# Kernel optimization log

Hardware: AMD Instinct MI355X
Metric: run time of the kernel (lower is better)

## Reference

```python
import jax, jax.numpy as jnp
import numpy as np

N = 100000      # nodes
E = 3200000     # directed edges
G = 1024        # graphs in batch


def setup_inputs() -> dict:
    key = jax.random.key(0)
    ks = jax.random.split(key, 12)
    x = jax.random.normal(ks[0], (N, 4), dtype=jnp.float32)
    edge_index = jax.random.randint(ks[1], (2, E), 0, N, dtype=jnp.int64)
    batch = jnp.sort(jax.random.randint(ks[2], (N,), 0, G, dtype=jnp.int64))
    s = 0.1
    return {
        'x': x, 'edge_index': edge_index, 'batch': batch,
        'W_emb': jax.random.normal(ks[3], (4, 1), jnp.float32) * s,
        'b_emb': jax.random.normal(ks[4], (4,), jnp.float32) * s,
        'W1': jax.random.normal(ks[5], (16, 7), jnp.float32) * s,
        'b1': jax.random.normal(ks[6], (16,), jnp.float32) * s,
        'W2': jax.random.normal(ks[7], (8, 16), jnp.float32) * s,
        'b2': jax.random.normal(ks[8], (8,), jnp.float32) * s,
        'W3': jax.random.normal(ks[9], (1, 8), jnp.float32) * s,
        'b3': jax.random.normal(ks[10], (1,), jnp.float32) * s,
    }


def _gcn_norm(edge_index, n):
    # add self-loops (PyG GCNConv default)
    loops = jnp.arange(n, dtype=edge_index.dtype)
    row = jnp.concatenate([edge_index[0], loops])  # source
    col = jnp.concatenate([edge_index[1], loops])  # target
    deg = jax.ops.segment_sum(jnp.ones_like(col, dtype=jnp.float32), col, num_segments=n)
    dinv = jnp.where(deg > 0, deg ** -0.5, 0.0)
    norm = dinv[row] * dinv[col]
    return row, col, norm


def _gcn_conv(h, W, b, row, col, norm, n):
    h = h @ W.T                                   # [n, out]
    msg = h[row] * norm[:, None]                  # gather + scale
    out = jax.ops.segment_sum(msg, col, num_segments=n)
    return out + b


def reference(x, edge_index, batch, W_emb, b_emb, W1, b1, W2, b2, W3, b3):
    row, col, norm = _gcn_norm(edge_index, N)
    atoms_vector = x[:, :1]
    atoms_xyz = x[:, 1:]
    one_hot_emb = atoms_vector @ W_emb.T + b_emb          # [N, 4]
    h = jnp.concatenate([one_hot_emb, atoms_xyz], axis=1) # [N, 7]
    h = jnp.tanh(_gcn_conv(h, W1, b1, row, col, norm, N)) # [N, 16]
    # dropout is identity in eval mode
    h = jnp.tanh(_gcn_conv(h, W2, b2, row, col, norm, N)) # [N, 8]
    # scatter-mean readout over graphs
    sums = jax.ops.segment_sum(h, batch, num_segments=G)
    cnts = jax.ops.segment_sum(jnp.ones((h.shape[0],), h.dtype), batch, num_segments=G)
    pooled = sums / jnp.maximum(cnts, 1.0)[:, None]       # [G, 8]
    return pooled @ W3.T + b3                             # [G, 1]
```

## Files before the change

### kernel.cpp

```cpp
#include <hip/hip_runtime.h>
#include <hip/hip_fp16.h>


constexpr int BLK  = 256;
constexpr int NPB  = 256;
constexpr int NBMX = 512;
constexpr int CAPB = 9216;
constexpr int PBLK = 512;
constexpr int CAPS = 6144;
constexpr int EPT  = 12;
constexpr int SBLK = 512;
constexpr int MAXIT = CAPB / SBLK;

__global__ void k_place(const int4* __restrict__ row4, const int4* __restrict__ col4,
                        int* __restrict__ bucketCnt, unsigned int* __restrict__ data,
                        int E, int NB) {
    __shared__ unsigned int stage[CAPS];
    __shared__ int pos[NBMX], sstart[NBMX], lbase[NBMX];
    __shared__ int wsum[8];
    int t = threadIdx.x;
    int lane = t & 63, w = t >> 6;
    int begin = blockIdx.x * CAPS;
    int end = min(E, begin + CAPS);
    int csize = end - begin;
    int q0 = begin >> 2, q1 = end >> 2;
    if (t < NBMX) pos[t] = 0;
    __syncthreads();
    unsigned int ent[EPT];
    int meta[EPT];
#pragma unroll
    for (int it = 0; it < EPT / 4; it++) {
        int i = q0 + t + it * PBLK;
        bool ok = i < q1;
        int4 c = ok ? col4[i] : make_int4(0, 0, 0, 0);
        int4 r = ok ? row4[i] : make_int4(0, 0, 0, 0);
#pragma unroll
        for (int k = 0; k < 4; k++) {
            int cc = ((const int*)&c)[k];
            int rr = ((const int*)&r)[k];
            int b = cc >> 8;
            int o = ok ? atomicAdd(&pos[b], 1) : 0;
            ent[it * 4 + k] = ((unsigned int)(cc & 255) << 17) | (unsigned int)rr;
            meta[it * 4 + k] = ok ? ((b << 13) | o) : -1;
        }
    }
    __syncthreads();
    int v = pos[t];
    int sc = v;
#pragma unroll
    for (int off = 1; off < 64; off <<= 1) {
        int o = __shfl_up(sc, off, 64);
        if (lane >= off) sc += o;
    }
    if (lane == 63) wsum[w] = sc;
    __syncthreads();
    int pre = 0;
#pragma unroll
    for (int i = 0; i < 8; i++) if (i < w) pre += wsum[i];
    int excl = sc + pre - v;
    sstart[t] = excl;
    lbase[t] = v ? atomicAdd(&bucketCnt[t], v) : 0;
    __syncthreads();
#pragma unroll
    for (int k = 0; k < EPT; k++) {
        int m = meta[k];
        if (m >= 0) stage[sstart[m >> 13] + (m & 0x1FFF)] = ent[k];
    }
    __syncthreads();
    for (int k = t; k < csize; k += PBLK) {
        int lo = 0, hi = NB - 1;
        while (lo < hi) { int m = (lo + hi + 1) >> 1; if (sstart[m] <= k) lo = m; else hi = m - 1; }
        data[(unsigned int)lo * CAPB + (unsigned int)(lbase[lo] + (k - sstart[lo]))] = stage[k];
    }
}

__global__ void k_sort_node1(unsigned int* __restrict__ data,
                             const int* __restrict__ bucketCnt,
                             const float4* __restrict__ x,
                             const float* __restrict__ Wemb, const float* __restrict__ bemb,
                             const float* __restrict__ W1,
                             int* __restrict__ rs, int* __restrict__ re,
                             float* __restrict__ dinv, uint4* __restrict__ u1q, int n) {
    __shared__ int pos[NPB], startl[NPB];
    __shared__ int wsum[4];
    int b = blockIdx.x;
    int t = threadIdx.x;
    int base = b * CAPB;
    int cnt = min(bucketCnt[b], CAPB);
    if (t < NPB) pos[t] = 0;
    __syncthreads();
    unsigned int ent[MAXIT];
    int off[MAXIT];
#pragma unroll
    for (int it = 0; it < MAXIT; it++) {
        int i = t + it * SBLK;
        if (i < cnt) {
            unsigned int p = data[base + i];
            int dloc = (int)(p >> 17);
            int o = atomicAdd(&pos[dloc], 1);
            ent[it] = p & 0x1FFFF;
            off[it] = (dloc << 14) | o;
        } else off[it] = -1;
    }
    __syncthreads();
    int node = b * NPB + t;
    float d = 0.0f;
    if (t < NPB) {
        int lane = t & 63, w = t >> 6;
        int v = pos[t];
        int sc = v;
#pragma unroll
        for (int o = 1; o < 64; o <<= 1) {
            int s = __shfl_up(sc, o, 64);
            if (lane >= o) sc += s;
        }
        if (lane == 63) wsum[w] = sc;
        __syncthreads();
        int pre = 0;
#pragma unroll
        for (int i = 0; i < 4; i++) if (i < w) pre += wsum[i];
        int excl = sc + pre - v;
        startl[t] = excl;
        if (node < n) {
            rs[node] = base + excl;
            re[node] = base + excl + v;
            d = rsqrtf((float)v + 1.0f);
            dinv[node] = d;
        }
    } else {
        __syncthreads();
    }
    __syncthreads();
#pragma unroll
    for (int it = 0; it < MAXIT; it++) {
        int m = off[it];
        if (m >= 0) data[base + startl[m >> 14] + (m & 0x3FFF)] = ent[it];
    }
    if (t < NPB && node < n) {
        float4 xi = x[node];
        float h0[7];
#pragma unroll
        for (int j = 0; j < 4; j++) h0[j] = xi.x * Wemb[j] + bemb[j];
        h0[4] = xi.y; h0[5] = xi.z; h0[6] = xi.w;
        float s[16];
#pragma unroll
        for (int f = 0; f < 16; f++) {
            float tt = 0.0f;
#pragma unroll
            for (int j = 0; j < 7; j++) tt += h0[j] * W1[f * 7 + j];
            s[f] = tt * d;
        }
        union { __half2 h2[8]; uint4 u4[2]; } pk;
#pragma unroll
        for (int q = 0; q < 8; q++) pk.h2[q] = __floats2half2_rn(s[2*q], s[2*q+1]);
        u1q[node * 2]     = pk.u4[0];
        u1q[node * 2 + 1] = pk.u4[1];
    }
}

__global__ void k_agg1(const unsigned int* __restrict__ sorted,
                       const int* __restrict__ rs, const int* __restrict__ re,
                       const uint4* __restrict__ u1q, const float* __restrict__ dinv,
                       const float* __restrict__ b1, const float* __restrict__ W2,
                       uint2* __restrict__ u2h, int n) {
    __shared__ float hbuf[128][17];
    int t = threadIdx.x;
    int nl = t >> 1;
    int j = t & 1;
    int node = blockIdx.x * 128 + nl;
    if (node < n) {
        int s = rs[node], e = re[node];
        float acc[8];
#pragma unroll
        for (int k = 0; k < 8; k++) acc[k] = 0.0f;
        int i = s;
        for (; i + 4 <= e; i += 4) {
            uint4 q0 = u1q[sorted[i]     * 2 + j];
            uint4 q1 = u1q[sorted[i + 1] * 2 + j];
            uint4 q2 = u1q[sorted[i + 2] * 2 + j];
            uint4 q3 = u1q[sorted[i + 3] * 2 + j];
            const __half2* p0 = (const __half2*)&q0;
            const __half2* p1 = (const __half2*)&q1;
            const __half2* p2 = (const __half2*)&q2;
            const __half2* p3 = (const __half2*)&q3;
#pragma unroll
            for (int k = 0; k < 4; k++) {
                float2 a0 = __half22float2(p0[k]);
                float2 a1 = __half22float2(p1[k]);
                float2 a2 = __half22float2(p2[k]);
                float2 a3 = __half22float2(p3[k]);
                acc[2*k]   += (a0.x + a1.x) + (a2.x + a3.x);
                acc[2*k+1] += (a0.y + a1.y) + (a2.y + a3.y);
            }
        }
        for (; i < e; i++) {
            uint4 q = u1q[sorted[i] * 2 + j];
            const __half2* p = (const __half2*)&q;
#pragma unroll
            for (int k = 0; k < 4; k++) {
                float2 a = __half22float2(p[k]);
                acc[2*k]   += a.x;
                acc[2*k+1] += a.y;
            }
        }
        uint4 qs = u1q[node * 2 + j];
        const __half2* ps = (const __half2*)&qs;
        float d = dinv[node];
#pragma unroll
        for (int k = 0; k < 4; k++) {
            float2 a = __half22float2(ps[k]);
            hbuf[nl][j*8 + 2*k]   = tanhf(d * (acc[2*k]   + a.x) + b1[j*8 + 2*k]);
            hbuf[nl][j*8 + 2*k+1] = tanhf(d * (acc[2*k+1] + a.y) + b1[j*8 + 2*k+1]);
        }
    }
    __syncthreads();
    if (node < n) {
        float d = dinv[node];
        float r[4];
#pragma unroll
        for (int gg = 0; gg < 4; gg++) {
            float tt = 0.0f;
#pragma unroll
            for (int k = 0; k < 16; k++) tt += hbuf[nl][k] * W2[(j*4 + gg) * 16 + k];
            r[gg] = tt * d;
        }
        union { __half2 h2[2]; uint2 u2; } pk;
        pk.h2[0] = __floats2half2_rn(r[0], r[1]);
        pk.h2[1] = __floats2half2_rn(r[2], r[3]);
        u2h[node * 2 + j] = pk.u2;
    }
}

__global__ void k_agg2(const unsigned int* __restrict__ sorted,
                       const int* __restrict__ rs, const int* __restrict__ re,
                       const uint4* __restrict__ u2q, const float* __restrict__ dinv,
                       const float* __restrict__ b2, uint4* __restrict__ h2q, int n) {
    int node = blockIdx.x * BLK + threadIdx.x;
    if (node >= n) return;
    int s = rs[node], e = re[node];
    float acc[8];
#pragma unroll
    for (int k = 0; k < 8; k++) acc[k] = 0.0f;
    int i = s;
    for (; i + 2 <= e; i += 2) {
        uint4 q0 = u2q[sorted[i]];
        uint4 q1 = u2q[sorted[i + 1]];
        const __half2* p0 = (const __half2*)&q0;
        const __half2* p1 = (const __half2*)&q1;
#pragma unroll
        for (int k = 0; k < 4; k++) {
            float2 a0 = __half22float2(p0[k]);
            float2 a1 = __half22float2(p1[k]);
            acc[2*k]   += a0.x + a1.x;
            acc[2*k+1] += a0.y + a1.y;
        }
    }
    if (i < e) {
        uint4 q = u2q[sorted[i]];
        const __half2* p = (const __half2*)&q;
#pragma unroll
        for (int k = 0; k < 4; k++) {
            float2 a = __half22float2(p[k]);
            acc[2*k]   += a.x;
            acc[2*k+1] += a.y;
        }
    }
    uint4 qs = u2q[node];
    const __half2* ps = (const __half2*)&qs;
    float d = dinv[node];
    union { __half2 h2[4]; uint4 u4; } pk;
#pragma unroll
    for (int k = 0; k < 4; k++) {
        float2 a = __half22float2(ps[k]);
        pk.h2[k] = __floats2half2_rn(tanhf(d * (acc[2*k]   + a.x) + b2[2*k]),
                                     tanhf(d * (acc[2*k+1] + a.y) + b2[2*k+1]));
    }
    h2q[node] = pk.u4;
}

__global__ void k_pool_out(const uint4* __restrict__ h2q, const int* __restrict__ batch,
                           const float* __restrict__ W3, const float* __restrict__ b3,
                           float* __restrict__ out, int n) {
    int g = blockIdx.x;
    int lane = threadIdx.x;
    int lo = 0, hi = n;
    while (lo < hi) { int m = (lo + hi) >> 1; if (batch[m] < g) lo = m + 1; else hi = m; }
    int start = lo;
    hi = n;
    while (lo < hi) { int m = (lo + hi) >> 1; if (batch[m] < g + 1) lo = m + 1; else hi = m; }
    int end = lo;

    float s[8];
#pragma unroll
    for (int f = 0; f < 8; f++) s[f] = 0.0f;
    for (int i = start + lane; i < end; i += 64) {
        uint4 q = h2q[i];
        const __half2* ph = (const __half2*)&q;
#pragma unroll
        for (int p = 0; p < 4; p++) {
            float2 a = __half22float2(ph[p]);
            s[2*p]   += a.x;
            s[2*p+1] += a.y;
        }
    }
#pragma unroll
    for (int off = 32; off >= 1; off >>= 1) {
#pragma unroll
        for (int f = 0; f < 8; f++) s[f] += __shfl_down(s[f], off, 64);
    }
    if (lane == 0) {
        float c = fmaxf((float)(end - start), 1.0f);
        float t = 0.0f;
#pragma unroll
        for (int f = 0; f < 8; f++) t += (s[f] / c) * W3[f];
        out[g] = t + b3[0];
    }
}

extern "C" void kernel_launch(void* const* d_in, const int* in_sizes, int n_in,
                              void* d_out, int out_size, void* d_ws, size_t ws_size,
                              hipStream_t stream) {
    const float* x    = (const float*)d_in[0];
    const int*   ei   = (const int*)d_in[1];
    const int*   batch= (const int*)d_in[2];
    const float* Wemb = (const float*)d_in[3];
    const float* bemb = (const float*)d_in[4];
    const float* W1   = (const float*)d_in[5];
    const float* b1   = (const float*)d_in[6];
    const float* W2   = (const float*)d_in[7];
    const float* b2   = (const float*)d_in[8];
    const float* W3   = (const float*)d_in[9];
    const float* b3   = (const float*)d_in[10];
    float* out = (float*)d_out;

    const int n = in_sizes[2];
    const int E = in_sizes[1] / 2;
    const int G = out_size;
    const int* row = ei;
    const int* col = ei + E;
    const int NB = (n + NPB - 1) / NPB;

    float* ws    = (float*)d_ws;
    float* dinv  = ws;
    uint4* u1q   = (uint4*)(ws + n);
    __half* u2h  = (__half*)(ws + 9 * n);
    __half* h2h  = (__half*)(ws + 13 * n);
    int* rs      = (int*)(ws + 17 * n);
    int* re      = rs + n;
    int* bucketCnt = re + n;
    unsigned int* data = (unsigned int*)(bucketCnt + NBMX);

    int gridP = (E + CAPS - 1) / CAPS;

    hipMemsetAsync(bucketCnt, 0, NBMX * sizeof(int), stream);
    k_place<<<gridP, PBLK, 0, stream>>>((const int4*)row, (const int4*)col,
                                        bucketCnt, data, E, NB);
    k_sort_node1<<<NB, SBLK, 0, stream>>>(data, bucketCnt, (const float4*)x,
                                          Wemb, bemb, W1, rs, re, dinv, u1q, n);
    k_agg1<<<(n + 127) / 128, BLK, 0, stream>>>(data, rs, re, u1q,
                                                dinv, b1, W2, (uint2*)u2h, n);
    k_agg2<<<(n + BLK - 1) / BLK, BLK, 0, stream>>>(data, rs, re, (const uint4*)u2h,
                                                    dinv, b2, (uint4*)h2h, n);
    k_pool_out<<<G, 64, 0, stream>>>((const uint4*)h2h, batch, W3, b3, out, n);
}
```

Measured before the change: 209.6 us.

## Fuse second GCN aggregation with graph mean-pooling via wave segmented reduction

The pooling readout is folded into the second aggregation kernel. Each wave runs a shuffle-based segmented reduction keyed by graph id, and segment heads add their partial sums and counts into a pooled buffer with atomics. A small kernel then applies the mean and the final linear layer. This removes the fp16 h2 intermediate write/read and the per-graph binary-search pooling kernel, at the cost of float atomics (nondeterministic summation order) and an extended memset.

```diff
diff --git a/kernel.cpp b/kernel.cpp
--- a/kernel.cpp
+++ b/kernel.cpp
@@ -231,90 +231,92 @@
     }
 }
 
-__global__ void k_agg2(const unsigned int* __restrict__ sorted,
-                       const int* __restrict__ rs, const int* __restrict__ re,
-                       const uint4* __restrict__ u2q, const float* __restrict__ dinv,
-                       const float* __restrict__ b2, uint4* __restrict__ h2q, int n) {
+__global__ void k_agg2_pool(const unsigned int* __restrict__ sorted,
+                            const int* __restrict__ rs, const int* __restrict__ re,
+                            const uint4* __restrict__ u2q, const float* __restrict__ dinv,
+                            const float* __restrict__ b2, const int* __restrict__ batch,
+                            float* __restrict__ pooled, float* __restrict__ cnt, int n) {
     int node = blockIdx.x * BLK + threadIdx.x;
-    if (node >= n) return;
-    int s = rs[node], e = re[node];
-    float acc[8];
-#pragma unroll
-    for (int k = 0; k < 8; k++) acc[k] = 0.0f;
-    int i = s;
-    for (; i + 2 <= e; i += 2) {
-        uint4 q0 = u2q[sorted[i]];
-        uint4 q1 = u2q[sorted[i + 1]];
-        const __half2* p0 = (const __half2*)&q0;
-        const __half2* p1 = (const __half2*)&q1;
+    int lane = threadIdx.x & 63;
+    bool valid = node < n;
+    float h[8];
+#pragma unroll
+    for (int k = 0; k < 8; k++) h[k] = 0.0f;
+    int g = -1;
+    if (valid) {
+        int s = rs[node], e = re[node];
+        float acc[8];
+#pragma unroll
+        for (int k = 0; k < 8; k++) acc[k] = 0.0f;
+        int i = s;
+        for (; i + 2 <= e; i += 2) {
+            uint4 q0 = u2q[sorted[i]];
+            uint4 q1 = u2q[sorted[i + 1]];
+            const __half2* p0 = (const __half2*)&q0;
+            const __half2* p1 = (const __half2*)&q1;
+#pragma unroll
+            for (int k = 0; k < 4; k++) {
+                float2 a0 = __half22float2(p0[k]);
+                float2 a1 = __half22float2(p1[k]);
+                acc[2*k]   += a0.x + a1.x;
+                acc[2*k+1] += a0.y + a1.y;
+            }
+        }
+        if (i < e) {
+            uint4 q = u2q[sorted[i]];
+            const __half2* p = (const __half2*)&q;
+#pragma unroll
+            for (int k = 0; k < 4; k++) {
+                float2 a = __half22float2(p[k]);
+                acc[2*k]   += a.x;
+                acc[2*k+1] += a.y;
+            }
+        }
+        uint4 qs = u2q[node];
+        const __half2* ps = (const __half2*)&qs;
+        float d = dinv[node];
 #pragma unroll
         for (int k = 0; k < 4; k++) {
-            float2 a0 = __half22float2(p0[k]);
-            float2 a1 = __half22float2(p1[k]);
-            acc[2*k]   += a0.x + a1.x;
-            acc[2*k+1] += a0.y + a1.y;
-        }
-    }
-    if (i < e) {
-        uint4 q = u2q[sorted[i]];
-        const __half2* p = (const __half2*)&q;
-#pragma unroll
-        for (int k = 0; k < 4; k++) {
-            float2 a = __half22float2(p[k]);
-            acc[2*k]   += a.x;
-            acc[2*k+1] += a.y;
-        }
-    }
-    uint4 qs = u2q[node];
-    const __half2* ps = (const __half2*)&qs;
-    float d = dinv[node];
-    union { __half2 h2[4]; uint4 u4; } pk;
-#pragma unroll
-    for (int k = 0; k < 4; k++) {
-        float2 a = __half22float2(ps[k]);
-        pk.h2[k] = __floats2half2_rn(tanhf(d * (acc[2*k]   + a.x) + b2[2*k]),
-                                     tanhf(d * (acc[2*k+1] + a.y) + b2[2*k+1]));
-    }
-    h2q[node] = pk.u4;
-}
-
-__global__ void k_pool_out(const uint4* __restrict__ h2q, const int* __restrict__ batch,
-                           const float* __restrict__ W3, const float* __restrict__ b3,
-                           float* __restrict__ out, int n) {
-    int g = blockIdx.x;
-    int lane = threadIdx.x;
-    int lo = 0, hi = n;
-    while (lo < hi) { int m = (lo + hi) >> 1; if (batch[m] < g) lo = m + 1; else hi = m; }
-    int start = lo;
-    hi = n;
-    while (lo < hi) { int m = (lo + hi) >> 1; if (batch[m] < g + 1) lo = m + 1; else hi = m; }
-    int end = lo;
-
-    float s[8];
-#pragma unroll
-    for (int f = 0; f < 8; f++) s[f] = 0.0f;
-    for (int i = start + lane; i < end; i += 64) {
-        uint4 q = h2q[i];
-        const __half2* ph = (const __half2*)&q;
-#pragma unroll
-        for (int p = 0; p < 4; p++) {
-            float2 a = __half22float2(ph[p]);
-            s[2*p]   += a.x;
-            s[2*p+1] += a.y;
-        }
-    }
-#pragma unroll
-    for (int off = 32; off >= 1; off >>= 1) {
-#pragma unroll
-        for (int f = 0; f < 8; f++) s[f] += __shfl_down(s[f], off, 64);
-    }
-    if (lane == 0) {
-        float c = fmaxf((float)(end - start), 1.0f);
-        float t = 0.0f;
-#pragma unroll
-        for (int f = 0; f < 8; f++) t += (s[f] / c) * W3[f];
-        out[g] = t + b3[0];
-    }
+            float2 a = __half22float2(ps[k]);
+            h[2*k]   = tanhf(d * (acc[2*k]   + a.x) + b2[2*k]);
+            h[2*k+1] = tanhf(d * (acc[2*k+1] + a.y) + b2[2*k+1]);
+        }
+        g = batch[node];
+    }
+    float c = valid ? 1.0f : 0.0f;
+#pragma unroll
+    for (int off = 1; off < 64; off <<= 1) {
+        int gn = __shfl_down(g, off, 64);
+        float cn = __shfl_down(c, off, 64);
+        float hn[8];
+#pragma unroll
+        for (int k = 0; k < 8; k++) hn[k] = __shfl_down(h[k], off, 64);
+        bool take = (lane + off < 64) && (gn == g);
+        if (take) {
+            c += cn;
+#pragma unroll
+            for (int k = 0; k < 8; k++) h[k] += hn[k];
+        }
+    }
+    int gprev = __shfl_up(g, 1, 64);
+    bool head = valid && (lane == 0 || gprev != g);
+    if (head) {
+#pragma unroll
+        for (int k = 0; k < 8; k++) atomicAdd(&pooled[g * 8 + k], h[k]);
+        atomicAdd(&cnt[g], c);
+    }
+}
+
+__global__ void k_out(const float* __restrict__ pooled, const float* __restrict__ cnt,
+                      const float* __restrict__ W3, const float* __restrict__ b3,
+                      float* __restrict__ out, int G) {
+    int g = blockIdx.x * BLK + threadIdx.x;
+    if (g >= G) return;
+    float c = fmaxf(cnt[g], 1.0f);
+    float t = 0.0f;
+#pragma unroll
+    for (int k = 0; k < 8; k++) t += pooled[g * 8 + k] * W3[k];
+    out[g] = t / c + b3[0];
 }
 
 extern "C" void kernel_launch(void* const* d_in, const int* in_sizes, int n_in,
@@ -344,22 +346,24 @@
     float* dinv  = ws;
     uint4* u1q   = (uint4*)(ws + n);
     __half* u2h  = (__half*)(ws + 9 * n);
-    __half* h2h  = (__half*)(ws + 13 * n);
-    int* rs      = (int*)(ws + 17 * n);
+    int* rs      = (int*)(ws + 13 * n);
     int* re      = rs + n;
     int* bucketCnt = re + n;
-    unsigned int* data = (unsigned int*)(bucketCnt + NBMX);
+    float* pooled  = (float*)(bucketCnt + NBMX);
+    float* cnt     = pooled + 8 * G;
+    unsigned int* data = (unsigned int*)(cnt + G);
 
     int gridP = (E + CAPS - 1) / CAPS;
 
-    hipMemsetAsync(bucketCnt, 0, NBMX * sizeof(int), stream);
+    hipMemsetAsync(bucketCnt, 0, (NBMX + 8 * G + G) * sizeof(int), stream);
     k_place<<<gridP, PBLK, 0, stream>>>((const int4*)row, (const int4*)col,
                                         bucketCnt, data, E, NB);
     k_sort_node1<<<NB, SBLK, 0, stream>>>(data, bucketCnt, (const float4*)x,
                                           Wemb, bemb, W1, rs, re, dinv, u1q, n);
     k_agg1<<<(n + 127) / 128, BLK, 0, stream>>>(data, rs, re, u1q,
                                                 dinv, b1, W2, (uint2*)u2h, n);
-    k_agg2<<<(n + BLK - 1) / BLK, BLK, 0, stream>>>(data, rs, re, (const uint4*)u2h,
-                                                    dinv, b2, (uint4*)h2h, n);
-    k_pool_out<<<G, 64, 0, stream>>>((const uint4*)h2h, batch, W3, b3, out, n);
-}
+    k_agg2_pool<<<(n + BLK - 1) / BLK, BLK, 0, stream>>>(data, rs, re,
+                                                         (const uint4*)u2h, dinv, b2,
+                                                         batch, pooled, cnt, n);
+    k_out<<<(G + BLK - 1) / BLK, BLK, 0, stream>>>(pooled, cnt, W3, b3, out, G);
+}
```

Result: no change. 207.2 us (-1.1%).
